# Kernel optimization log

Measured on AMD Instinct MI355X. Metric: run time of the kernel, lower is better.

## Reference

```python
import jax, jax.numpy as jnp
import numpy as np

EPS = 1e-12  # torch F.normalize eps


def _l2_normalize(x):
    # matches torch.nn.functional.normalize(x, p=2, dim=-1)
    n = jnp.sqrt(jnp.sum(x * x, axis=-1, keepdims=True))
    return x / jnp.maximum(n, EPS)


def setup_inputs() -> dict:
    key = jax.random.key(0)
    k1, k2 = jax.random.split(key)
    b, i, m, kdim = 4, 25, 128, 64
    query = jax.random.normal(k1, (b, i, m, kdim), dtype=jnp.float32)
    support = jax.random.normal(k2, (b, i, m, kdim), dtype=jnp.float32)
    return {"query": query, "support": support}


def reference(query, support):
    """RelationGenerator.forward with way='cosine', mask=False.

    query:   [b, i, m, k]
    support: [b, j, n, k]
    returns: [b, i, j, m, n] cosine similarity matrix
    """
    qn = _l2_normalize(query)
    sn = _l2_normalize(support)
    # per-batch einsum 'imk,jnk->ijmn', stacked over b
    return jnp.einsum("bimk,bjnk->bijmn", qn, sn)
```

## Files before the change

kernel.cpp:

```cpp
#include <hip/hip_runtime.h>

typedef unsigned short u16;
typedef unsigned int u32;
typedef __attribute__((ext_vector_type(8))) short short8;
typedef __attribute__((ext_vector_type(4))) float floatx4;
typedef __attribute__((ext_vector_type(4))) u32 uint4v;

__device__ __forceinline__ u32 pack2bf(float a, float b) {
    u32 ua = __float_as_uint(a), ub = __float_as_uint(b);
    ua += 0x7fffu + ((ua >> 16) & 1u);
    ub += 0x7fffu + ((ub >> 16) & 1u);
    return __builtin_amdgcn_perm(ub, ua, 0x07060302);
}

__global__ __launch_bounds__(256)
void normalize_pack_kernel(const float* __restrict__ q,
                           const float* __restrict__ s,
                           u16* __restrict__ ws)
{
    const int t      = threadIdx.x;
    const int blk    = blockIdx.x;
    const int tensor = blk / 100;
    const int tile   = blk % 100;

    const float* src = (tensor ? s : q) + (size_t)tile * 8192;
    u16*         dst = ws + (size_t)blk * 8192;

    const int row  = t >> 1;
    const int half = t & 1;
    const float* gp = src + row * 64 + half * 32;

    float4 f[8];
#pragma unroll
    for (int c = 0; c < 8; ++c) f[c] = ((const float4*)gp)[c];
    float ss = 0.f;
#pragma unroll
    for (int c = 0; c < 8; ++c)
        ss += f[c].x*f[c].x + f[c].y*f[c].y + f[c].z*f[c].z + f[c].w*f[c].w;
    ss += __shfl_xor(ss, 1);
    const float r = 1.0f / fmaxf(sqrtf(ss), 1e-12f);

    u16* base = dst + ((size_t)((row >> 4) * 2 + half) * 512) + (row & 15) * 8;
#pragma unroll
    for (int c = 0; c < 4; ++c) {
        uint4v pk;
        pk.x = pack2bf(f[2*c].x * r,   f[2*c].y * r);
        pk.y = pack2bf(f[2*c].z * r,   f[2*c].w * r);
        pk.z = pack2bf(f[2*c+1].x * r, f[2*c+1].y * r);
        pk.w = pack2bf(f[2*c+1].z * r, f[2*c+1].w * r);
        *(uint4v*)(base + c * 128) = pk;
    }
}

__global__ __launch_bounds__(256, 4)
void cosine_gemm_kernel(const u16* __restrict__ ws,
                        float* __restrict__ out)
{
    const int t   = threadIdx.x;
    const int blk = blockIdx.x;
    const int b   = blk / 625;
    const int rem = blk % 625;
    const int i   = rem / 25;
    const int j   = rem % 25;

    const u16* qtile = ws + (size_t)(b * 25 + i) * 8192;
    const u16* stile = ws + (size_t)(100 + b * 25 + j) * 8192;

    const int wave = t >> 6;
    const int lane = t & 63;
    const int quad = lane >> 4;
    const int l15  = lane & 15;
    const int m0   = (wave >> 1) * 64;
    const int n0   = (wave & 1) * 64;

    floatx4 acc[4][4] = {};
#pragma unroll
    for (int ks = 0; ks < 2; ++ks) {
        short8 af[4], bfr[4];
#pragma unroll
        for (int mt = 0; mt < 4; ++mt)
            af[mt] = *(const short8*)(qtile +
                      (size_t)(((m0 >> 4) + mt) * 2 + ks) * 512 + lane * 8);
#pragma unroll
        for (int nt = 0; nt < 4; ++nt)
            bfr[nt] = *(const short8*)(stile +
                      (size_t)(((n0 >> 4) + nt) * 2 + ks) * 512 + lane * 8);
#pragma unroll
        for (int mt = 0; mt < 4; ++mt)
#pragma unroll
            for (int nt = 0; nt < 4; ++nt)
                acc[mt][nt] = __builtin_amdgcn_mfma_f32_16x16x32_bf16(
                    af[mt], bfr[nt], acc[mt][nt], 0, 0, 0);
    }

    float* obase = out + (size_t)blk * 16384 + n0 + l15;
#pragma unroll
    for (int mt = 0; mt < 4; ++mt) {
#pragma unroll
        for (int r = 0; r < 4; ++r) {
            float* op = obase + (size_t)(m0 + mt * 16 + quad * 4 + r) * 128;
#pragma unroll
            for (int nt = 0; nt < 4; ++nt)
                op[nt * 16] = acc[mt][nt][r];
        }
    }
}

#define QPITCH 72

__global__ __launch_bounds__(256, 4)
void cosine_relation_kernel(const float* __restrict__ q,
                            const float* __restrict__ s,
                            float* __restrict__ out)
{
    __shared__ u16 smem[2 * 128 * QPITCH];
    u16* qt = smem;
    u16* st = smem + 128 * QPITCH;

    const int t   = threadIdx.x;
    const int blk = blockIdx.x;
    const int b   = blk / 625;
    const int rem = blk % 625;
    const int i   = rem / 25;
    const int j   = rem % 25;

    const float* qbase = q + (size_t)(b * 25 + i) * 8192;
    const float* sbase = s + (size_t)(b * 25 + j) * 8192;

    const int row  = t >> 1;
    const int half = t & 1;
#pragma unroll
    for (int tile = 0; tile < 2; ++tile) {
        const float* gp = (tile == 0 ? qbase : sbase) + row * 64 + half * 32;
        u16*         lp = (tile == 0 ? qt : st) + row * QPITCH + half * 32;
        float4 f[8];
#pragma unroll
        for (int c = 0; c < 8; ++c) f[c] = ((const float4*)gp)[c];
        float ss = 0.f;
#pragma unroll
        for (int c = 0; c < 8; ++c)
            ss += f[c].x*f[c].x + f[c].y*f[c].y + f[c].z*f[c].z + f[c].w*f[c].w;
        ss += __shfl_xor(ss, 1);
        const float r = 1.0f / fmaxf(sqrtf(ss), 1e-12f);
#pragma unroll
        for (int c = 0; c < 4; ++c) {
            uint4v pk;
            pk.x = pack2bf(f[2*c].x * r,   f[2*c].y * r);
            pk.y = pack2bf(f[2*c].z * r,   f[2*c].w * r);
            pk.z = pack2bf(f[2*c+1].x * r, f[2*c+1].y * r);
            pk.w = pack2bf(f[2*c+1].z * r, f[2*c+1].w * r);
            *(uint4v*)(lp + c * 8) = pk;
        }
    }
    __syncthreads();

    const int wave = t >> 6;
    const int lane = t & 63;
    const int quad = lane >> 4;
    const int l15  = lane & 15;
    const int m0   = (wave >> 1) * 64;
    const int n0   = (wave & 1) * 64;

    floatx4 acc[4][4] = {};
#pragma unroll
    for (int ks = 0; ks < 2; ++ks) {
        short8 af[4], bfr[4];
#pragma unroll
        for (int mt = 0; mt < 4; ++mt)
            af[mt] = *(const short8*)(qt + (m0 + mt * 16 + l15) * QPITCH + ks * 32 + quad * 8);
#pragma unroll
        for (int nt = 0; nt < 4; ++nt)
            bfr[nt] = *(const short8*)(st + (n0 + nt * 16 + l15) * QPITCH + ks * 32 + quad * 8);
#pragma unroll
        for (int mt = 0; mt < 4; ++mt)
#pragma unroll
            for (int nt = 0; nt < 4; ++nt)
                acc[mt][nt] = __builtin_amdgcn_mfma_f32_16x16x32_bf16(
                    af[mt], bfr[nt], acc[mt][nt], 0, 0, 0);
    }

    float* obase = out + (size_t)blk * 16384 + n0 + l15;
#pragma unroll
    for (int mt = 0; mt < 4; ++mt) {
#pragma unroll
        for (int r = 0; r < 4; ++r) {
            float* op = obase + (size_t)(m0 + mt * 16 + quad * 4 + r) * 128;
#pragma unroll
            for (int nt = 0; nt < 4; ++nt)
                op[nt * 16] = acc[mt][nt][r];
        }
    }
}

extern "C" void kernel_launch(void* const* d_in, const int* in_sizes, int n_in,
                              void* d_out, int out_size, void* d_ws, size_t ws_size,
                              hipStream_t stream) {
    const float* q = (const float*)d_in[0];
    const float* s = (const float*)d_in[1];
    float* out = (float*)d_out;

    const size_t WS_NEED = (size_t)200 * 16384;
    if (d_ws != nullptr && ws_size >= WS_NEED) {
        normalize_pack_kernel<<<200, 256, 0, stream>>>(q, s, (u16*)d_ws);
        cosine_gemm_kernel<<<2500, 256, 0, stream>>>((const u16*)d_ws, out);
    } else {
        cosine_relation_kernel<<<2500, 256, 0, stream>>>(q, s, out);
    }
}
```

Baseline: 169.0 us.

## Fuse normalize and GEMM into one cooperative persistent kernel with grid sync

Result: slower. 294.4 us (+74.2%).

```diff
diff --git a/kernel.cpp b/kernel.cpp
--- a/kernel.cpp
+++ b/kernel.cpp
@@ -1,4 +1,7 @@
 #include <hip/hip_runtime.h>
+#include <hip/hip_cooperative_groups.h>
+
+namespace cg = cooperative_groups;
 
 typedef unsigned short u16;
 typedef unsigned int u32;
@@ -13,16 +16,13 @@
     return __builtin_amdgcn_perm(ub, ua, 0x07060302);
 }
 
-__global__ __launch_bounds__(256)
-void normalize_pack_kernel(const float* __restrict__ q,
-                           const float* __restrict__ s,
-                           u16* __restrict__ ws)
-{
-    const int t      = threadIdx.x;
-    const int blk    = blockIdx.x;
+__device__ __forceinline__ void normalize_tile(const float* __restrict__ q,
+                                               const float* __restrict__ s,
+                                               u16* __restrict__ ws,
+                                               int blk, int t)
+{
     const int tensor = blk / 100;
     const int tile   = blk % 100;
-
     const float* src = (tensor ? s : q) + (size_t)tile * 8192;
     u16*         dst = ws + (size_t)blk * 8192;
 
@@ -52,19 +52,58 @@
     }
 }
 
-__global__ __launch_bounds__(256, 4)
-void cosine_gemm_kernel(const u16* __restrict__ ws,
-                        float* __restrict__ out)
-{
-    const int t   = threadIdx.x;
-    const int blk = blockIdx.x;
-    const int b   = blk / 625;
-    const int rem = blk % 625;
+struct Frags { short8 a[2][4]; short8 b[2][4]; };
+
+__device__ __forceinline__ void load_frags(Frags& F, const u16* __restrict__ ws,
+                                           int tidx, int m0, int n0, int lane)
+{
+    const int b   = tidx / 625;
+    const int rem = tidx % 625;
     const int i   = rem / 25;
     const int j   = rem % 25;
-
-    const u16* qtile = ws + (size_t)(b * 25 + i) * 8192;
-    const u16* stile = ws + (size_t)(100 + b * 25 + j) * 8192;
+    const u16* qt = ws + (size_t)(b * 25 + i) * 8192;
+    const u16* st = ws + (size_t)(100 + b * 25 + j) * 8192;
+#pragma unroll
+    for (int ks = 0; ks < 2; ++ks) {
+#pragma unroll
+        for (int mt = 0; mt < 4; ++mt)
+            F.a[ks][mt] = *(const short8*)(qt +
+                          (size_t)(((m0 >> 4) + mt) * 2 + ks) * 512 + lane * 8);
+#pragma unroll
+        for (int nt = 0; nt < 4; ++nt)
+            F.b[ks][nt] = *(const short8*)(st +
+                          (size_t)(((n0 >> 4) + nt) * 2 + ks) * 512 + lane * 8);
+    }
+}
+
+__device__ __forceinline__ void store_tile(float* __restrict__ out, int tidx,
+                                           const floatx4 acc[4][4],
+                                           int m0, int n0, int quad, int l15)
+{
+    float* obase = out + (size_t)tidx * 16384 + n0 + l15;
+#pragma unroll
+    for (int mt = 0; mt < 4; ++mt)
+#pragma unroll
+        for (int r = 0; r < 4; ++r) {
+            float* op = obase + (size_t)(m0 + mt * 16 + quad * 4 + r) * 128;
+#pragma unroll
+            for (int nt = 0; nt < 4; ++nt)
+                op[nt * 16] = acc[mt][nt][r];
+        }
+}
+
+__global__ __launch_bounds__(256, 2)
+void fused_cosine_kernel(const float* __restrict__ q,
+                         const float* __restrict__ s,
+                         u16* __restrict__ ws,
+                         float* __restrict__ out)
+{
+    const int blk = blockIdx.x;
+    const int t   = threadIdx.x;
+
+    if (blk < 200) normalize_tile(q, s, ws, blk, t);
+    __threadfence();
+    cg::this_grid().sync();
 
     const int wave = t >> 6;
     const int lane = t & 63;
@@ -73,37 +112,63 @@
     const int m0   = (wave >> 1) * 64;
     const int n0   = (wave & 1) * 64;
 
+    Frags cur;
+    load_frags(cur, ws, blk, m0, n0, lane);
+
+#pragma unroll
+    for (int it = 0; it < 5; ++it) {
+        const int tc = blk + it * 512;
+        if (tc >= 2500) break;
+        floatx4 acc[4][4] = {};
+#pragma unroll
+        for (int ks = 0; ks < 2; ++ks)
+#pragma unroll
+            for (int mt = 0; mt < 4; ++mt)
+#pragma unroll
+                for (int nt = 0; nt < 4; ++nt)
+                    acc[mt][nt] = __builtin_amdgcn_mfma_f32_16x16x32_bf16(
+                        cur.a[ks][mt], cur.b[ks][nt], acc[mt][nt], 0, 0, 0);
+        const int tn = tc + 512;
+        Frags nxt;
+        if (tn < 2500) load_frags(nxt, ws, tn, m0, n0, lane);
+        store_tile(out, tc, acc, m0, n0, quad, l15);
+        if (tn < 2500) cur = nxt;
+    }
+}
+
+__global__ __launch_bounds__(256)
+void normalize_pack_kernel(const float* __restrict__ q,
+                           const float* __restrict__ s,
+                           u16* __restrict__ ws)
+{
+    normalize_tile(q, s, ws, blockIdx.x, threadIdx.x);
+}
+
+__global__ __launch_bounds__(256, 4)
+void cosine_gemm_kernel(const u16* __restrict__ ws,
+                        float* __restrict__ out)
+{
+    const int t   = threadIdx.x;
+    const int blk = blockIdx.x;
+    const int wave = t >> 6;
+    const int lane = t & 63;
+    const int quad = lane >> 4;
+    const int l15  = lane & 15;
+    const int m0   = (wave >> 1) * 64;
+    const int n0   = (wave & 1) * 64;
+
+    Frags F;
+    load_frags(F, ws, blk, m0, n0, lane);
     floatx4 acc[4][4] = {};
 #pragma unroll
-    for (int ks = 0; ks < 2; ++ks) {
-        short8 af[4], bfr[4];
-#pragma unroll
-        for (int mt = 0; mt < 4; ++mt)
-            af[mt] = *(const short8*)(qtile +
-                      (size_t)(((m0 >> 4) + mt) * 2 + ks) * 512 + lane * 8);
-#pragma unroll
-        for (int nt = 0; nt < 4; ++nt)
-            bfr[nt] = *(const short8*)(stile +
-                      (size_t)(((n0 >> 4) + nt) * 2 + ks) * 512 + lane * 8);
+    for (int ks = 0; ks < 2; ++ks)
 #pragma unroll
         for (int mt = 0; mt < 4; ++mt)
 #pragma unroll
             for (int nt = 0; nt < 4; ++nt)
                 acc[mt][nt] = __builtin_amdgcn_mfma_f32_16x16x32_bf16(
-                    af[mt], bfr[nt], acc[mt][nt], 0, 0, 0);
-    }
-
-    float* obase = out + (size_t)blk * 16384 + n0 + l15;
-#pragma unroll
-    for (int mt = 0; mt < 4; ++mt) {
-#pragma unroll
-        for (int r = 0; r < 4; ++r) {
-            float* op = obase + (size_t)(m0 + mt * 16 + quad * 4 + r) * 128;
-#pragma unroll
-            for (int nt = 0; nt < 4; ++nt)
-                op[nt * 16] = acc[mt][nt][r];
-        }
-    }
+                    F.a[ks][mt], F.b[ks][nt], acc[mt][nt], 0, 0, 0);
+    store_tile(out, blk, acc, m0, n0, quad, l15);
 }
 
 #define QPITCH 72
@@ -181,7 +246,7 @@
 
     float* obase = out + (size_t)blk * 16384 + n0 + l15;
 #pragma unroll
-    for (int mt = 0; mt < 4; ++mt) {
+    for (int mt = 0; mt < 4; ++mt)
 #pragma unroll
         for (int r = 0; r < 4; ++r) {
             float* op = obase + (size_t)(m0 + mt * 16 + quad * 4 + r) * 128;
@@ -189,7 +254,6 @@
             for (int nt = 0; nt < 4; ++nt)
                 op[nt * 16] = acc[mt][nt][r];
         }
-    }
 }
 
 extern "C" void kernel_launch(void* const* d_in, const int* in_sizes, int n_in,
@@ -201,8 +265,15 @@
 
     const size_t WS_NEED = (size_t)200 * 16384;
     if (d_ws != nullptr && ws_size >= WS_NEED) {
-        normalize_pack_kernel<<<200, 256, 0, stream>>>(q, s, (u16*)d_ws);
-        cosine_gemm_kernel<<<2500, 256, 0, stream>>>((const u16*)d_ws, out);
+        u16* ws = (u16*)d_ws;
+        void* args[] = { (void*)&q, (void*)&s, (void*)&ws, (void*)&out };
+        hipError_t e = hipLaunchCooperativeKernel(
+            (const void*)fused_cosine_kernel, dim3(512), dim3(256),
+            args, 0, stream);
+        if (e == hipSuccess) return;
+        (void)hipGetLastError();
+        normalize_pack_kernel<<<200, 256, 0, stream>>>(q, s, ws);
+        cosine_gemm_kernel<<<2500, 256, 0, stream>>>(ws, out);
     } else {
         cosine_relation_kernel<<<2500, 256, 0, stream>>>(q, s, out);
     }
```
